# Kernel optimization log

Measured on AMD Instinct MI355X. Metric: run time of the kernel, lower is better.

The kernel has to match this reference:

```python
import jax, jax.numpy as jnp
import numpy as np

B, S, D, F, E, TOP_K = 2, 2048, 1024, 2048, 8, 2


def setup_inputs() -> dict:
    key = jax.random.key(0)
    k0, k1, k2, k3 = jax.random.split(key, 4)
    return {
        "hidden_states": jax.random.normal(k0, (B, S, D), jnp.float32),
        "gate_w": jax.random.normal(k1, (E, D), jnp.float32) * 0.02,   # torch Linear weight [out=E, in=D]
        "w1": jax.random.normal(k2, (E, D, F), jnp.float32) * 0.02,    # per-expert up-proj
        "w2": jax.random.normal(k3, (E, F, D), jnp.float32) * 0.02,    # per-expert down-proj
    }


def reference(hidden_states, gate_w, w1, w2):
    b, s, d = hidden_states.shape
    e = gate_w.shape[0]
    x = hidden_states.reshape(-1, d)                 # [T, D]
    t = x.shape[0]
    router_logits = x @ gate_w.T                     # [T, E]
    # softmax in fp32 as in original, then renormalized top-k weights
    probs = jax.nn.softmax(router_logits.astype(jnp.float32), axis=-1)
    topw, sel = jax.lax.top_k(probs, TOP_K)          # [T, K]
    topw = topw / jnp.sum(topw, axis=-1, keepdims=True)
    topw = topw.astype(x.dtype)
    # dense combine weights: zero for unselected experts (top_k indices are distinct)
    combine = jnp.zeros((t, e), x.dtype).at[jnp.arange(t)[:, None], sel].add(topw)  # [T, E]
    out = jnp.zeros_like(x)
    for ei in range(e):  # small fixed expert count
        h = jax.nn.silu(x @ w1[ei]) @ w2[ei]         # [T, D]
        out = out + combine[:, ei:ei + 1] * h
    return out.reshape(b, s, d), router_logits
```

## Files before the change

kernel.cpp:

```cpp
#include <hip/hip_runtime.h>
#include <hip/hip_bf16.h>
#include <math.h>

#define Tt 4096
#define Dd 1024
#define Ff 2048
#define Ee 8

typedef unsigned short u16;
typedef short bf16x8 __attribute__((ext_vector_type(8)));
typedef float f32x4 __attribute__((ext_vector_type(4)));

__device__ __forceinline__ u16 f2bf(float f) {
  union { float f; unsigned u; } v; v.f = f;
  unsigned r = v.u + 0x7fffu + ((v.u >> 16) & 1u);
  return (u16)(r >> 16);
}

__device__ __forceinline__ void gload16(const void* g, void* l) {
  __builtin_amdgcn_global_load_lds(
      (const __attribute__((address_space(1))) unsigned int*)g,
      (__attribute__((address_space(3))) unsigned int*)l, 16, 0, 0);
}

__global__ __launch_bounds__(256) void router_kernel(
    const float* __restrict__ x, const float* __restrict__ gw,
    float* __restrict__ logits, u16* __restrict__ xb)
{
  int t = blockIdx.x * 4 + (threadIdx.x >> 6);
  int lane = threadIdx.x & 63;
  const float* xr = x + (size_t)t * Dd;
  float xv[16];
#pragma unroll
  for (int i = 0; i < 4; ++i) {
    float4 v = *reinterpret_cast<const float4*>(xr + lane * 16 + i * 4);
    xv[i*4+0] = v.x; xv[i*4+1] = v.y; xv[i*4+2] = v.z; xv[i*4+3] = v.w;
  }
  if (xb) {
#pragma unroll
    for (int i = 0; i < 4; ++i) {
      ushort4 b;
      b.x = f2bf(xv[i*4+0]); b.y = f2bf(xv[i*4+1]);
      b.z = f2bf(xv[i*4+2]); b.w = f2bf(xv[i*4+3]);
      *reinterpret_cast<ushort4*>(xb + (size_t)t * Dd + lane * 16 + i * 4) = b;
    }
  }
#pragma unroll
  for (int e = 0; e < Ee; ++e) {
    const float* gr = gw + (size_t)e * Dd + lane * 16;
    float s = 0.f;
#pragma unroll
    for (int i = 0; i < 4; ++i) {
      float4 g = *reinterpret_cast<const float4*>(gr + i * 4);
      s += xv[i*4+0]*g.x + xv[i*4+1]*g.y + xv[i*4+2]*g.z + xv[i*4+3]*g.w;
    }
#pragma unroll
    for (int o = 32; o > 0; o >>= 1) s += __shfl_xor(s, o);
    if (lane == 0) logits[(size_t)t * Ee + e] = s;
  }
}

__global__ __launch_bounds__(256) void build_kernel(
    const float* __restrict__ logits, int* __restrict__ meta,
    int* __restrict__ list, float* __restrict__ wgt)
{
  __shared__ int hist[8], cur[8];
  const int tid = threadIdx.x;
  const int lane = tid & 63;
  if (tid < 8) hist[tid] = 0;
  __syncthreads();
  for (int it = 0; it < Tt / 256; ++it) {
    int t = it * 256 + tid;
    float4 lo = *reinterpret_cast<const float4*>(logits + (size_t)t * 8);
    float4 hi = *reinterpret_cast<const float4*>(logits + (size_t)t * 8 + 4);
    float s[8] = {lo.x, lo.y, lo.z, lo.w, hi.x, hi.y, hi.z, hi.w};
    int i1 = 0; float m1 = s[0];
#pragma unroll
    for (int e = 1; e < 8; ++e) if (s[e] > m1) { m1 = s[e]; i1 = e; }
    int i2 = -1; float m2 = -__builtin_inff();
#pragma unroll
    for (int e = 0; e < 8; ++e) if (e != i1 && s[e] > m2) { m2 = s[e]; i2 = e; }
#pragma unroll
    for (int k = 0; k < 2; ++k) {
      int gg = k ? i2 : i1;
      unsigned long long m = ~0ull;
#pragma unroll
      for (int b = 0; b < 3; ++b) {
        unsigned long long vb = __ballot((gg >> b) & 1);
        m &= ((gg >> b) & 1) ? vb : ~vb;
      }
      int rank = __popcll(m & ((1ull << lane) - 1));
      if (rank == 0) atomicAdd(&hist[gg], __popcll(m));
    }
  }
  __syncthreads();
  if (tid == 0) {
    int sacc = 0;
    for (int g = 0; g < 8; ++g) {
      meta[g] = hist[g];
      meta[32 + g] = sacc;
      cur[g] = sacc;
      sacc += hist[g];
    }
  }
  __syncthreads();
  for (int it = 0; it < Tt / 256; ++it) {
    int t = it * 256 + tid;
    float4 lo = *reinterpret_cast<const float4*>(logits + (size_t)t * 8);
    float4 hi = *reinterpret_cast<const float4*>(logits + (size_t)t * 8 + 4);
    float s[8] = {lo.x, lo.y, lo.z, lo.w, hi.x, hi.y, hi.z, hi.w};
    int i1 = 0; float m1 = s[0];
#pragma unroll
    for (int e = 1; e < 8; ++e) if (s[e] > m1) { m1 = s[e]; i1 = e; }
    int i2 = -1; float m2 = -__builtin_inff();
#pragma unroll
    for (int e = 0; e < 8; ++e) if (e != i1 && s[e] > m2) { m2 = s[e]; i2 = e; }
    float wa = 1.f / (1.f + expf(m2 - m1));
#pragma unroll
    for (int k = 0; k < 2; ++k) {
      int gg = k ? i2 : i1;
      float w = k ? (1.f - wa) : wa;
      unsigned long long m = ~0ull;
#pragma unroll
      for (int b = 0; b < 3; ++b) {
        unsigned long long vb = __ballot((gg >> b) & 1);
        m &= ((gg >> b) & 1) ? vb : ~vb;
      }
      int rank = __popcll(m & ((1ull << lane) - 1));
      int ldr = __ffsll(m) - 1;
      int base = 0;
      if (rank == 0) base = atomicAdd(&cur[gg], __popcll(m));
      base = __shfl(base, ldr);
      list[base + rank] = t;
      wgt[base + rank] = w;
    }
  }
}

__global__ __launch_bounds__(256) void transpose_bf16_kernel(
    const float* __restrict__ in, u16* __restrict__ out, int R, int C)
{
  __shared__ u16 st[64][65];
  const size_t eoff = (size_t)blockIdx.z * R * C;
  const float* ip = in + eoff;
  u16* op = out + eoff;
  int r0 = blockIdx.y * 64, c0 = blockIdx.x * 64;
  int t = threadIdx.x;
  int rr = t >> 2;
  int cb = (t & 3) * 16;
#pragma unroll
  for (int i = 0; i < 4; ++i) {
    float4 v = *reinterpret_cast<const float4*>(ip + (size_t)(r0 + rr) * C + c0 + cb + i * 4);
    st[rr][cb + i*4 + 0] = f2bf(v.x);
    st[rr][cb + i*4 + 1] = f2bf(v.y);
    st[rr][cb + i*4 + 2] = f2bf(v.z);
    st[rr][cb + i*4 + 3] = f2bf(v.w);
  }
  __syncthreads();
#pragma unroll
  for (int i = 0; i < 4; ++i) {
    ushort4 b;
    b.x = st[cb + i*4 + 0][rr];
    b.y = st[cb + i*4 + 1][rr];
    b.z = st[cb + i*4 + 2][rr];
    b.w = st[cb + i*4 + 3][rr];
    *reinterpret_cast<ushort4*>(op + (size_t)(c0 + rr) * R + r0 + cb + i * 4) = b;
  }
}

template<int MODE, int N_, int K_>
__global__ __launch_bounds__(256) void gemm_g(
    const u16* __restrict__ Abase, const u16* __restrict__ Bbase,
    void* __restrict__ Cout, const int* __restrict__ meta,
    const int* __restrict__ list, const float* __restrict__ wgt)
{
  constexpr int NXc = N_ / 128;
  constexpr int NYc = 32;
  constexpr int CPX = NXc * NYc;
  constexpr int ABUF = 128 * 32, BBUF = 128 * 32;
  constexpr int NT  = K_ / 32;

  __shared__ u16 Al[2 * ABUF];
  __shared__ u16 Bl[2 * BBUF];

  const int orig = blockIdx.x + NXc * (blockIdx.y + NYc * blockIdx.z);
  const int swz  = (orig & 7) * CPX + (orig >> 3);
  const int bz   = swz / (NXc * NYc);
  const int rem  = swz - bz * (NXc * NYc);
  const int by   = rem / NXc;
  const int bx   = rem - by * NXc;

  const int e   = bz;
  const int cnt = meta[e];
  if (by * 128 >= cnt) return;
  const int off = meta[32 + e];

  const int tid  = threadIdx.x;
  const int lane = tid & 63;
  const int wave = tid >> 6;
  const int wr   = wave >> 1, wc = wave & 1;
  const int n0   = bx * 128;

  const int l4 = lane >> 2;
  const int kp = (((lane & 3) ^ ((lane >> 3) & 3))) * 8;

  const u16* aptr[2];
  u16* alds[2];
#pragma unroll
  for (int c = 0; c < 2; ++c) {
    int chunk = wave * 2 + c;
    int row = chunk * 16 + l4;
    int i = by * 128 + row;
    if (i >= cnt) i = cnt - 1;
    int srow = (MODE == 0) ? list[off + i] : (off + i);
    aptr[c] = Abase + (size_t)srow * K_ + kp;
    alds[c] = Al + chunk * 512;
  }
  const u16* bptr[2];
  u16* blds[2];
#pragma unroll
  for (int c = 0; c < 2; ++c) {
    int chunk = wave * 2 + c;
    int row = chunk * 16 + l4;
    bptr[c] = Bbase + ((size_t)e * N_ + n0 + row) * K_ + kp;
    blds[c] = Bl + chunk * 512;
  }

  f32x4 acc[4][4] = {};
  const int r16 = lane & 15;
  const int kqs = (((lane >> 4) ^ ((lane >> 1) & 3))) * 8;

#pragma unroll
  for (int c = 0; c < 2; ++c) gload16(aptr[c], alds[c]);
#pragma unroll
  for (int c = 0; c < 2; ++c) gload16(bptr[c], blds[c]);
  __syncthreads();

  int cur = 0;
  for (int t = 0; t < NT; ++t) {
    if (t + 1 < NT) {
      int k0 = (t + 1) * 32;
      int nb = cur ^ 1;
#pragma unroll
      for (int c = 0; c < 2; ++c) gload16(aptr[c] + k0, alds[c] + nb * ABUF);
#pragma unroll
      for (int c = 0; c < 2; ++c) gload16(bptr[c] + k0, blds[c] + nb * BBUF);
    }
    const u16* Ab = Al + cur * ABUF;
    const u16* Bb = Bl + cur * BBUF;
    bf16x8 af[4], bfv[4];
#pragma unroll
    for (int m = 0; m < 4; ++m)
      af[m] = *reinterpret_cast<const bf16x8*>(&Ab[(wr*64 + m*16 + r16) * 32 + kqs]);
#pragma unroll
    for (int n = 0; n < 4; ++n)
      bfv[n] = *reinterpret_cast<const bf16x8*>(&Bb[(wc*64 + n*16 + r16) * 32 + kqs]);
#pragma unroll
    for (int m = 0; m < 4; ++m)
#pragma unroll
      for (int n = 0; n < 4; ++n)
        acc[m][n] = __builtin_amdgcn_mfma_f32_16x16x32_bf16(af[m], bfv[n], acc[m][n], 0, 0, 0);
    __syncthreads();
    cur ^= 1;
  }

  const int colb = n0 + wc * 64 + r16;
  const int rb4  = wr * 64 + ((lane >> 4) << 2);
#pragma unroll
  for (int m = 0; m < 4; ++m) {
#pragma unroll
    for (int r = 0; r < 4; ++r) {
      int i = by * 128 + rb4 + m * 16 + r;
      if (i >= cnt) continue;
      if (MODE == 0) {
        u16* hp = (u16*)Cout + (size_t)(off + i) * N_;
#pragma unroll
        for (int n = 0; n < 4; ++n) {
          float v = acc[m][n][r];
          v = v / (1.f + expf(-v));
          hp[colb + n * 16] = f2bf(v);
        }
      } else {
        int   tok = list[off + i];
        float w   = wgt[off + i];
        float* o = (float*)Cout + (size_t)tok * N_;
#pragma unroll
        for (int n = 0; n < 4; ++n)
          atomicAdd(&o[colb + n * 16], w * acc[m][n][r]);
      }
    }
  }
}

__global__ __launch_bounds__(256) void combine_kernel(
    const float* __restrict__ logits, float* __restrict__ combine)
{
  int t = blockIdx.x * 256 + threadIdx.x;
  if (t >= Tt) return;
  float4 lo = *reinterpret_cast<const float4*>(logits + (size_t)t * 8);
  float4 hi = *reinterpret_cast<const float4*>(logits + (size_t)t * 8 + 4);
  float s[8] = {lo.x, lo.y, lo.z, lo.w, hi.x, hi.y, hi.z, hi.w};
  int i1 = 0; float m1 = s[0];
#pragma unroll
  for (int e = 1; e < 8; ++e) if (s[e] > m1) { m1 = s[e]; i1 = e; }
  int i2 = -1; float m2 = -__builtin_inff();
#pragma unroll
  for (int e = 0; e < 8; ++e) if (e != i1 && s[e] > m2) { m2 = s[e]; i2 = e; }
  float wa = 1.f / (1.f + expf(m2 - m1));
#pragma unroll
  for (int e = 0; e < 8; ++e)
    combine[(size_t)t * 8 + e] = (e == i1) ? wa : ((e == i2) ? (1.f - wa) : 0.f);
}

template<int MODE, int N_, int K_>
__global__ __launch_bounds__(256) void gemm_dense(
    const float* __restrict__ A, const float* __restrict__ Bg,
    float* __restrict__ C, const float* __restrict__ combine,
    int expert, int first)
{
  constexpr int BM = 128, BN = 128, BK = 32, LDT = 40;
  __shared__ u16 Al[BM * LDT];
  __shared__ u16 Bl[BN * LDT];
  const int tid  = threadIdx.x;
  const int lane = tid & 63;
  const int wave = tid >> 6;
  const int wr = wave >> 1, wc = wave & 1;
  const int m0 = blockIdx.y * BM;
  const int n0 = blockIdx.x * BN;
  f32x4 acc[4][4] = {};
  for (int k0 = 0; k0 < K_; k0 += BK) {
#pragma unroll
    for (int i = 0; i < 4; ++i) {
      int f = tid + 256 * i;
      int row = f >> 3;
      int c4 = (f & 7) << 2;
      float4 v = *reinterpret_cast<const float4*>(A + (size_t)(m0 + row) * K_ + k0 + c4);
      ushort4 b;
      b.x = f2bf(v.x); b.y = f2bf(v.y); b.z = f2bf(v.z); b.w = f2bf(v.w);
      *reinterpret_cast<ushort4*>(&Al[row * LDT + c4]) = b;
    }
    {
      int n  = tid & 127;
      int kb = (tid >> 7) << 4;
      const float* bp = Bg + (size_t)(k0 + kb) * N_ + n0 + n;
      u16 tmp[16];
#pragma unroll
      for (int kk = 0; kk < 16; ++kk)
        tmp[kk] = f2bf(bp[(size_t)kk * N_]);
      u16* p = &Bl[n * LDT + kb];
#pragma unroll
      for (int i = 0; i < 4; ++i) {
        ushort4 b;
        b.x = tmp[i*4+0]; b.y = tmp[i*4+1]; b.z = tmp[i*4+2]; b.w = tmp[i*4+3];
        *reinterpret_cast<ushort4*>(p + i * 4) = b;
      }
    }
    __syncthreads();
    bf16x8 af[4], bfr[4];
    const int kq  = (lane >> 4) << 3;
    const int r16 = lane & 15;
#pragma unroll
    for (int m = 0; m < 4; ++m)
      af[m] = *reinterpret_cast<const bf16x8*>(&Al[(wr*64 + m*16 + r16) * LDT + kq]);
#pragma unroll
    for (int n = 0; n < 4; ++n)
      bfr[n] = *reinterpret_cast<const bf16x8*>(&Bl[(wc*64 + n*16 + r16) * LDT + kq]);
#pragma unroll
    for (int m = 0; m < 4; ++m)
#pragma unroll
      for (int n = 0; n < 4; ++n)
        acc[m][n] = __builtin_amdgcn_mfma_f32_16x16x32_bf16(af[m], bfr[n], acc[m][n], 0, 0, 0);
    __syncthreads();
  }
  const int col0 = n0 + wc * 64 + (lane & 15);
  const int rbs  = m0 + wr * 64 + ((lane >> 4) << 2);
#pragma unroll
  for (int m = 0; m < 4; ++m) {
#pragma unroll
    for (int r = 0; r < 4; ++r) {
      int row = rbs + m * 16 + r;
      if (MODE == 0) {
#pragma unroll
        for (int n = 0; n < 4; ++n) {
          float v = acc[m][n][r];
          v = v / (1.f + expf(-v));
          C[(size_t)row * N_ + col0 + n * 16] = v;
        }
      } else {
        float w = combine[(size_t)row * Ee + expert];
        if (first) {
#pragma unroll
          for (int n = 0; n < 4; ++n)
            C[(size_t)row * N_ + col0 + n * 16] = w * acc[m][n][r];
        } else {
#pragma unroll
          for (int n = 0; n < 4; ++n)
            C[(size_t)row * N_ + col0 + n * 16] += w * acc[m][n][r];
        }
      }
    }
  }
}

extern "C" void kernel_launch(void* const* d_in, const int* in_sizes, int n_in,
                              void* d_out, int out_size, void* d_ws, size_t ws_size,
                              hipStream_t stream)
{
  const float* x  = (const float*)d_in[0];
  const float* gw = (const float*)d_in[1];
  const float* w1 = (const float*)d_in[2];
  const float* w2 = (const float*)d_in[3];
  float* out    = (float*)d_out;
  float* logits = out + (size_t)Tt * Dd;

  int*   meta = (int*)d_ws;
  int*   list = (int*)((char*)d_ws + 256);
  float* wgt  = (float*)((char*)d_ws + 256 + 32768);
  u16*   xb   = (u16*)((char*)d_ws + 262144);
  u16*   h1   = (u16*)((char*)d_ws + 262144 + 8388608);
  u16*   wT   = (u16*)((char*)d_ws + 262144 + 8388608 + 33554432);
  const size_t NEED = 262144ull + 8388608ull + 33554432ull + 33554432ull;

  if (ws_size >= NEED) {
    router_kernel<<<Tt / 4, 256, 0, stream>>>(x, gw, logits, xb);
    hipMemsetAsync(out, 0, (size_t)Tt * Dd * sizeof(float), stream);
    build_kernel<<<1, 256, 0, stream>>>(logits, meta, list, wgt);
    transpose_bf16_kernel<<<dim3(Ff/64, Dd/64, Ee), 256, 0, stream>>>(w1, wT, Dd, Ff);
    gemm_g<0, Ff, Dd><<<dim3(Ff/128, 32, 8), 256, 0, stream>>>(xb, wT, h1, meta, list, wgt);
    transpose_bf16_kernel<<<dim3(Dd/64, Ff/64, Ee), 256, 0, stream>>>(w2, wT, Ff, Dd);
    gemm_g<1, Dd, Ff><<<dim3(Dd/128, 32, 8), 256, 0, stream>>>(h1, wT, out, meta, list, wgt);
  } else {
    float* combine = (float*)d_ws;
    float* h1d     = combine + (size_t)Tt * Ee;
    router_kernel<<<Tt / 4, 256, 0, stream>>>(x, gw, logits, nullptr);
    combine_kernel<<<Tt / 256, 256, 0, stream>>>(logits, combine);
    size_t cb = (size_t)Tt * Ee * sizeof(float);
    size_t avail = ws_size > cb ? (ws_size - cb) : 0;
    long maxrows = (long)(avail / ((size_t)Ff * sizeof(float)));
    int chunk = (maxrows >= Tt) ? Tt : (int)((maxrows / 128) * 128);
    if (chunk < 128) chunk = 128;
    for (int c0 = 0; c0 < Tt; c0 += chunk) {
      int rows = (Tt - c0) < chunk ? (Tt - c0) : chunk;
      for (int e = 0; e < Ee; ++e) {
        gemm_dense<0, Ff, Dd><<<dim3(Ff/128, rows/128), 256, 0, stream>>>(
            x + (size_t)c0 * Dd, w1 + (size_t)e * Dd * Ff, h1d, nullptr, e, 0);
        gemm_dense<1, Dd, Ff><<<dim3(Dd/128, rows/128), 256, 0, stream>>>(
            h1d, w2 + (size_t)e * Ff * Dd, out + (size_t)c0 * Dd,
            combine + (size_t)c0 * Ee, e, (e == 0) ? 1 : 0);
      }
    }
  }
}
```

Measured before the change: 213.4 us.

## Triple-buffer LDS in grouped GEMM with explicit vmcnt waits and single barrier

The grouped expert GEMM moves from double to triple LDS buffering, keeping two K-tiles of global-to-LDS loads in flight. A partial s_waitcnt vmcnt(4) plus one barrier per iteration replaces the prefetch-then-__syncthreads pattern, and s_setprio raises wave priority around the MFMA block. The aim is to hide global load latency better and drop one barrier per K step. LDS use per block grows by half, which may lower occupancy, and the hand-written waitcnt count depends on the compiler issuing exactly four loads per stage.

```diff
diff --git a/kernel.cpp b/kernel.cpp
--- a/kernel.cpp
+++ b/kernel.cpp
@@ -177,11 +177,11 @@
   constexpr int NXc = N_ / 128;
   constexpr int NYc = 32;
   constexpr int CPX = NXc * NYc;
-  constexpr int ABUF = 128 * 32, BBUF = 128 * 32;
+  constexpr int ABUF = 128 * 32;
   constexpr int NT  = K_ / 32;
 
-  __shared__ u16 Al[2 * ABUF];
-  __shared__ u16 Bl[2 * BBUF];
+  __shared__ u16 Al[3 * ABUF];
+  __shared__ u16 Bl[3 * ABUF];
 
   const int orig = blockIdx.x + NXc * (blockIdx.y + NYc * blockIdx.z);
   const int swz  = (orig & 7) * CPX + (orig >> 3);
@@ -205,7 +205,7 @@
   const int kp = (((lane & 3) ^ ((lane >> 3) & 3))) * 8;
 
   const u16* aptr[2];
-  u16* alds[2];
+  int aoff[2];
 #pragma unroll
   for (int c = 0; c < 2; ++c) {
     int chunk = wave * 2 + c;
@@ -214,54 +214,58 @@
     if (i >= cnt) i = cnt - 1;
     int srow = (MODE == 0) ? list[off + i] : (off + i);
     aptr[c] = Abase + (size_t)srow * K_ + kp;
-    alds[c] = Al + chunk * 512;
+    aoff[c] = chunk * 512;
   }
   const u16* bptr[2];
-  u16* blds[2];
+  int boff[2];
 #pragma unroll
   for (int c = 0; c < 2; ++c) {
     int chunk = wave * 2 + c;
     int row = chunk * 16 + l4;
     bptr[c] = Bbase + ((size_t)e * N_ + n0 + row) * K_ + kp;
-    blds[c] = Bl + chunk * 512;
+    boff[c] = chunk * 512;
   }
 
   f32x4 acc[4][4] = {};
   const int r16 = lane & 15;
   const int kqs = (((lane >> 4) ^ ((lane >> 1) & 3))) * 8;
 
-#pragma unroll
-  for (int c = 0; c < 2; ++c) gload16(aptr[c], alds[c]);
-#pragma unroll
-  for (int c = 0; c < 2; ++c) gload16(bptr[c], blds[c]);
-  __syncthreads();
-
-  int cur = 0;
+  u16 *a0 = Al, *a1 = Al + ABUF, *a2 = Al + 2 * ABUF;
+  u16 *b0 = Bl, *b1 = Bl + ABUF, *b2 = Bl + 2 * ABUF;
+
+#pragma unroll
+  for (int c = 0; c < 2; ++c) { gload16(aptr[c], a0 + aoff[c]); gload16(bptr[c], b0 + boff[c]); }
+#pragma unroll
+  for (int c = 0; c < 2; ++c) { gload16(aptr[c] + 32, a1 + aoff[c]); gload16(bptr[c] + 32, b1 + boff[c]); }
+
   for (int t = 0; t < NT; ++t) {
-    if (t + 1 < NT) {
-      int k0 = (t + 1) * 32;
-      int nb = cur ^ 1;
-#pragma unroll
-      for (int c = 0; c < 2; ++c) gload16(aptr[c] + k0, alds[c] + nb * ABUF);
-#pragma unroll
-      for (int c = 0; c < 2; ++c) gload16(bptr[c] + k0, blds[c] + nb * BBUF);
-    }
-    const u16* Ab = Al + cur * ABUF;
-    const u16* Bb = Bl + cur * BBUF;
+    if (t + 1 < NT) asm volatile("s_waitcnt vmcnt(4)" ::: "memory");
+    else            asm volatile("s_waitcnt vmcnt(0)" ::: "memory");
+    __builtin_amdgcn_s_barrier();
+
+    if (t + 2 < NT) {
+      int k0 = (t + 2) * 32;
+#pragma unroll
+      for (int c = 0; c < 2; ++c) { gload16(aptr[c] + k0, a2 + aoff[c]); gload16(bptr[c] + k0, b2 + boff[c]); }
+    }
+
     bf16x8 af[4], bfv[4];
 #pragma unroll
     for (int m = 0; m < 4; ++m)
-      af[m] = *reinterpret_cast<const bf16x8*>(&Ab[(wr*64 + m*16 + r16) * 32 + kqs]);
+      af[m] = *reinterpret_cast<const bf16x8*>(&a0[(wr*64 + m*16 + r16) * 32 + kqs]);
 #pragma unroll
     for (int n = 0; n < 4; ++n)
-      bfv[n] = *reinterpret_cast<const bf16x8*>(&Bb[(wc*64 + n*16 + r16) * 32 + kqs]);
+      bfv[n] = *reinterpret_cast<const bf16x8*>(&b0[(wc*64 + n*16 + r16) * 32 + kqs]);
+    __builtin_amdgcn_s_setprio(1);
 #pragma unroll
     for (int m = 0; m < 4; ++m)
 #pragma unroll
       for (int n = 0; n < 4; ++n)
         acc[m][n] = __builtin_amdgcn_mfma_f32_16x16x32_bf16(af[m], bfv[n], acc[m][n], 0, 0, 0);
-    __syncthreads();
-    cur ^= 1;
+    __builtin_amdgcn_s_setprio(0);
+
+    u16* ta = a0; a0 = a1; a1 = a2; a2 = ta;
+    u16* tb = b0; b0 = b1; b1 = b2; b2 = tb;
   }
 
   const int colb = n0 + wc * 64 + r16;
```

New measurement: 207.2 us. 1.03x faster.
